# Kernel tuning notes

Measured on AMD Instinct MI355X. Metric: run time of the kernel, lower is better.

The kernel has to match this reference:

```python
import jax, jax.numpy as jnp
import numpy as np

B, T, C, K, TNEI = 16, 1024, 1024, 8, 2
H = int(C * 1.5)  # FeedForward hidden = int(1.5*in_dim)
EPS = 1e-5


def setup_inputs() -> dict:
    key = jax.random.key(0)
    ks = jax.random.split(key, 16)
    ws = C ** -0.5  # fan-in style init scale for projections
    return {
        "x": jax.random.normal(ks[0], (B, T, C), jnp.float32),
        "radj": jax.random.uniform(ks[1], (B, T, K), jnp.float32),
        "inxs": jax.random.randint(ks[2], (B, T, K), 0, T),
        "Wq": jax.random.normal(ks[3], (C, C), jnp.float32) * ws,
        "Wk": jax.random.normal(ks[4], (C, C), jnp.float32) * ws,
        "Wv": jax.random.normal(ks[5], (C, C), jnp.float32) * ws,
        "Wo": jax.random.normal(ks[6], (C, C), jnp.float32) * ws,
        "ln1_g": jnp.ones((C,), jnp.float32),
        "ln1_b": jnp.zeros((C,), jnp.float32),
        "W1": jax.random.normal(ks[7], (C, H), jnp.float32) * ws,
        "b1": jnp.zeros((H,), jnp.float32),
        "W2": jax.random.normal(ks[8], (H, C), jnp.float32) * (H ** -0.5),
        "b2": jnp.zeros((C,), jnp.float32),
        "ln2_g": jnp.ones((C,), jnp.float32),
        "ln2_b": jnp.zeros((C,), jnp.float32),
    }


def _layernorm(x, g, b):
    mu = jnp.mean(x, axis=-1, keepdims=True)
    var = jnp.mean(jnp.square(x - mu), axis=-1, keepdims=True)
    return (x - mu) * jax.lax.rsqrt(var + EPS) * g + b


def reference(x, radj, inxs, Wq, Wk, Wv, Wo, ln1_g, ln1_b, W1, b1, W2, b2, ln2_g, ln2_b):
    scale = 1.0 / jnp.sqrt(jnp.asarray(C, x.dtype))
    gather = jax.vmap(lambda a, i: a[i])  # (T,C),(T,K) -> (T,K,C), vmapped over B

    # MBasicReason: tnei hops of top-k neighbor attention (adjacency-biased)
    h = x
    for _ in range(TNEI):
        q = h @ Wq                                  # (B,T,C)
        kn = gather(h @ Wk, inxs)                   # (B,T,K,C)
        vn = gather(h @ Wv, inxs)                   # (B,T,K,C)
        scores = jnp.einsum('btc,btkc->btk', q, kn) * scale + radj
        attn = jax.nn.softmax(scores, axis=-1)      # (B,T,K); dropout off (eval)
        h = jnp.einsum('btk,btkc->btc', attn, vn) @ Wo

    # residual + LN, FFN, residual + LN
    y = _layernorm(x + jax.nn.relu(h), ln1_g, ln1_b)
    f = jax.nn.relu(y @ W1 + b1) @ W2 + b2
    return _layernorm(y + f, ln2_g, ln2_b)
```

## Files before the change

### kernel.cpp

```cpp
#include <hip/hip_runtime.h>
#include <hip/hip_bf16.h>
#include <cstddef>
#include <cstdint>

#define B_    16
#define T_    1024
#define C_    1024
#define K_    8
#define H_    1536
#define TNEI_ 2
static constexpr float EPS_ = 1e-5f;

typedef __attribute__((ext_vector_type(8))) short bf16x8;
typedef __attribute__((ext_vector_type(4))) float f32x4;

__device__ __forceinline__ float bf2f(unsigned short u) {
    return __uint_as_float(((unsigned)u) << 16);
}
__device__ __forceinline__ unsigned short f2bf(float f) {
    __hip_bfloat16 h = __float2bfloat16(f);
    union { __hip_bfloat16 h; unsigned short u; } cvt;
    cvt.h = h;
    return cvt.u;
}

__device__ __forceinline__ void gload_lds16(const void* g, void* l) {
    __builtin_amdgcn_global_load_lds(
        (const __attribute__((address_space(1))) void*)g,
        (__attribute__((address_space(3))) void*)l,
        16, 0, 0);
}

__global__ __launch_bounds__(256) void f2bf_kernel(
    const float* __restrict__ in, unsigned short* __restrict__ out)
{
    const size_t i = (size_t)blockIdx.x * 256 + threadIdx.x;
    const float4 v = *reinterpret_cast<const float4*>(&in[i * 4]);
    ushort4 o;
    o.x = f2bf(v.x); o.y = f2bf(v.y); o.z = f2bf(v.z); o.w = f2bf(v.w);
    *reinterpret_cast<ushort4*>(&out[i * 4]) = o;
}

__global__ __launch_bounds__(256) void wtrans_kernel(
    const float* __restrict__ W, unsigned short* __restrict__ WT, int R, int Cc)
{
    __shared__ float t[32][33];
    const int c0 = blockIdx.x * 32, r0 = blockIdx.y * 32;
    const int tx = threadIdx.x & 31, ty = threadIdx.x >> 5;
    #pragma unroll
    for (int i = 0; i < 4; ++i)
        t[ty + 8 * i][tx] = W[(size_t)(r0 + ty + 8 * i) * Cc + c0 + tx];
    __syncthreads();
    #pragma unroll
    for (int i = 0; i < 4; ++i)
        WT[(size_t)(c0 + ty + 8 * i) * R + r0 + tx] = f2bf(t[tx][ty + 8 * i]);
}

template <int OUT_BF16, int BIAS, int RELU>
__global__ __launch_bounds__(256) void gemm_bt_kernel(
    const unsigned short* __restrict__ A, const unsigned short* __restrict__ Bt,
    const float* __restrict__ bias, void* __restrict__ Cout,
    int M, int N, int K)
{
    constexpr int BM = 128, BN = 128, BK = 32;
    __shared__ unsigned short smem[2 * (BM * BK + BN * BK)];

    const int tid  = threadIdx.x;
    const int lane = tid & 63;
    const int wid  = tid >> 6;
    const int wm   = wid >> 1, wn = wid & 1;

    const int nwg  = gridDim.x * gridDim.y;
    int bidl = blockIdx.y * gridDim.x + blockIdx.x;
    bidl = (bidl & 7) * (nwg >> 3) + (bidl >> 3);
    const int bx = bidl % gridDim.x;
    const int by = bidl / gridDim.x;
    const int row0 = by * BM;
    const int col0 = bx * BN;

    const int sub = lane >> 2;
    const int kch = lane & 3;

    f32x4 acc[4][4] = {};

    auto stage = [&](int buf, int kt) {
        unsigned short* As = smem + buf * 8192;
        unsigned short* Bs = As + 4096;
        #pragma unroll
        for (int i = 0; i < 2; ++i) {
            const int chunk = i * 4 + wid;
            const int r = chunk * 16 + sub;
            gload_lds16(&A[(size_t)(row0 + r) * K + kt + kch * 8], &As[chunk * 512]);
        }
        #pragma unroll
        for (int i = 0; i < 2; ++i) {
            const int chunk = i * 4 + wid;
            const int r = chunk * 16 + sub;
            gload_lds16(&Bt[(size_t)(col0 + r) * K + kt + kch * 8], &Bs[chunk * 512]);
        }
    };

    auto compute = [&](int buf) {
        const unsigned short* As = smem + buf * 8192;
        const unsigned short* Bs = As + 4096;
        bf16x8 a[4], b[4];
        #pragma unroll
        for (int m = 0; m < 4; ++m) {
            const int r = wm * 64 + m * 16 + (lane & 15);
            a[m] = *reinterpret_cast<const bf16x8*>(&As[r * 32 + (lane >> 4) * 8]);
        }
        #pragma unroll
        for (int n = 0; n < 4; ++n) {
            const int c = wn * 64 + n * 16 + (lane & 15);
            b[n] = *reinterpret_cast<const bf16x8*>(&Bs[c * 32 + (lane >> 4) * 8]);
        }
        #pragma unroll
        for (int m = 0; m < 4; ++m)
            #pragma unroll
            for (int n = 0; n < 4; ++n)
                acc[m][n] = __builtin_amdgcn_mfma_f32_16x16x32_bf16(
                    a[m], b[n], acc[m][n], 0, 0, 0);
    };

    stage(0, 0);
    asm volatile("s_waitcnt vmcnt(0)" ::: "memory");
    __syncthreads();
    int cur = 0;
    for (int kt = BK; kt < K; kt += BK) {
        stage(cur ^ 1, kt);
        compute(cur);
        asm volatile("s_waitcnt vmcnt(0)" ::: "memory");
        __syncthreads();
        cur ^= 1;
    }
    compute(cur);

    if (OUT_BF16) {
        __syncthreads();
        char* tile = (char*)smem;
        #pragma unroll
        for (int m = 0; m < 4; ++m) {
            #pragma unroll
            for (int n = 0; n < 4; ++n) {
                const int cc = wn * 64 + n * 16 + (lane & 15);
                const float bv = BIAS ? bias[col0 + cc] : 0.0f;
                #pragma unroll
                for (int r = 0; r < 4; ++r) {
                    const int rr = wm * 64 + m * 16 + (lane >> 4) * 4 + r;
                    float v = acc[m][n][r] + bv;
                    if (RELU) v = fmaxf(v, 0.0f);
                    const int byte = (rr * 256 + cc * 2) ^ (((rr >> 2) & 3) << 5);
                    *reinterpret_cast<unsigned short*>(tile + byte) = f2bf(v);
                }
            }
        }
        __syncthreads();
        const int cchunk = tid & 15;
        const int rloc   = tid >> 4;
        #pragma unroll
        for (int p = 0; p < 8; ++p) {
            const int rr = p * 16 + rloc;
            const int byte = (rr * 256 + cchunk * 16) ^ (((rr >> 2) & 3) << 5);
            const uint4 v = *reinterpret_cast<const uint4*>(tile + byte);
            *reinterpret_cast<uint4*>(
                &((unsigned short*)Cout)[(size_t)(row0 + rr) * N + col0 + cchunk * 8]) = v;
        }
    } else {
        #pragma unroll
        for (int m = 0; m < 4; ++m) {
            #pragma unroll
            for (int n = 0; n < 4; ++n) {
                const int cg = col0 + wn * 64 + n * 16 + (lane & 15);
                const float bv = BIAS ? bias[cg] : 0.0f;
                #pragma unroll
                for (int r = 0; r < 4; ++r) {
                    const int rg = row0 + wm * 64 + m * 16 + (lane >> 4) * 4 + r;
                    float v = acc[m][n][r] + bv;
                    if (RELU) v = fmaxf(v, 0.0f);
                    ((float*)Cout)[(size_t)rg * N + cg] = v;
                }
            }
        }
    }
}

__global__ __launch_bounds__(256) void attn_kernel(
    const unsigned short* __restrict__ q, const unsigned short* __restrict__ kbuf,
    const unsigned short* __restrict__ vbuf, const int* __restrict__ inxs,
    const float* __restrict__ radj, unsigned short* __restrict__ out)
{
    const int bt  = blockIdx.x;
    const int b   = bt >> 10;
    const int tid = threadIdx.x;
    const float scale = 0.03125f;

    __shared__ int   s_idx[K_];
    __shared__ float s_sc[K_];
    __shared__ float red[K_][4];

    if (tid < K_) s_idx[tid] = inxs[bt * K_ + tid];
    __syncthreads();

    const ushort4 qv = *reinterpret_cast<const ushort4*>(&q[(size_t)bt * C_ + tid * 4]);
    const float qf[4] = { bf2f(qv.x), bf2f(qv.y), bf2f(qv.z), bf2f(qv.w) };

    float part[K_];
    #pragma unroll
    for (int k = 0; k < K_; ++k) {
        const size_t nb = (size_t)b * T_ + s_idx[k];
        const ushort4 kv = *reinterpret_cast<const ushort4*>(&kbuf[nb * C_ + tid * 4]);
        part[k] = qf[0] * bf2f(kv.x) + qf[1] * bf2f(kv.y)
                + qf[2] * bf2f(kv.z) + qf[3] * bf2f(kv.w);
    }

    const int lane = tid & 63, wid = tid >> 6;
    #pragma unroll
    for (int k = 0; k < K_; ++k) {
        float v = part[k];
        #pragma unroll
        for (int off = 32; off; off >>= 1) v += __shfl_xor(v, off);
        if (lane == 0) red[k][wid] = v;
    }
    __syncthreads();
    if (tid < K_) {
        s_sc[tid] = (red[tid][0] + red[tid][1] + red[tid][2] + red[tid][3]) * scale
                    + radj[bt * K_ + tid];
    }
    __syncthreads();

    float m = s_sc[0];
    #pragma unroll
    for (int k = 1; k < K_; ++k) m = fmaxf(m, s_sc[k]);
    float w[K_], wsum = 0.f;
    #pragma unroll
    for (int k = 0; k < K_; ++k) { w[k] = expf(s_sc[k] - m); wsum += w[k]; }
    const float inv = 1.0f / wsum;

    float o[4] = {0.f, 0.f, 0.f, 0.f};
    #pragma unroll
    for (int k = 0; k < K_; ++k) {
        const size_t nb = (size_t)b * T_ + s_idx[k];
        const ushort4 vv = *reinterpret_cast<const ushort4*>(&vbuf[nb * C_ + tid * 4]);
        const float wk = w[k] * inv;
        o[0] = fmaf(wk, bf2f(vv.x), o[0]);
        o[1] = fmaf(wk, bf2f(vv.y), o[1]);
        o[2] = fmaf(wk, bf2f(vv.z), o[2]);
        o[3] = fmaf(wk, bf2f(vv.w), o[3]);
    }
    ushort4 ov;
    ov.x = f2bf(o[0]); ov.y = f2bf(o[1]); ov.z = f2bf(o[2]); ov.w = f2bf(o[3]);
    *reinterpret_cast<ushort4*>(&out[(size_t)bt * C_ + tid * 4]) = ov;
}

template <int RELU, int WB>
__global__ __launch_bounds__(256) void ln_residual_kernel(
    const float* __restrict__ a, const float* __restrict__ bb,
    const float* __restrict__ g, const float* __restrict__ beta,
    float* __restrict__ out, unsigned short* __restrict__ outb)
{
    const int bt  = blockIdx.x;
    const int tid = threadIdx.x;

    const float4 av = *reinterpret_cast<const float4*>(&a[(size_t)bt * C_ + tid * 4]);
    const float4 bv = *reinterpret_cast<const float4*>(&bb[(size_t)bt * C_ + tid * 4]);
    float4 s;
    s.x = av.x + (RELU ? fmaxf(bv.x, 0.f) : bv.x);
    s.y = av.y + (RELU ? fmaxf(bv.y, 0.f) : bv.y);
    s.z = av.z + (RELU ? fmaxf(bv.z, 0.f) : bv.z);
    s.w = av.w + (RELU ? fmaxf(bv.w, 0.f) : bv.w);

    float sum = s.x + s.y + s.z + s.w;
    float sq  = s.x * s.x + s.y * s.y + s.z * s.z + s.w * s.w;

    const int lane = tid & 63, wid = tid >> 6;
    __shared__ float rs[4], rq[4];
    #pragma unroll
    for (int off = 32; off; off >>= 1) {
        sum += __shfl_xor(sum, off);
        sq  += __shfl_xor(sq,  off);
    }
    if (lane == 0) { rs[wid] = sum; rq[wid] = sq; }
    __syncthreads();
    sum = rs[0] + rs[1] + rs[2] + rs[3];
    sq  = rq[0] + rq[1] + rq[2] + rq[3];

    const float mu  = sum * (1.0f / C_);
    const float var = sq * (1.0f / C_) - mu * mu;
    const float r   = rsqrtf(var + EPS_);

    const float4 gv = *reinterpret_cast<const float4*>(&g[tid * 4]);
    const float4 be = *reinterpret_cast<const float4*>(&beta[tid * 4]);
    float4 o;
    o.x = (s.x - mu) * r * gv.x + be.x;
    o.y = (s.y - mu) * r * gv.y + be.y;
    o.z = (s.z - mu) * r * gv.z + be.z;
    o.w = (s.w - mu) * r * gv.w + be.w;
    *reinterpret_cast<float4*>(&out[(size_t)bt * C_ + tid * 4]) = o;
    if (WB) {
        ushort4 ob;
        ob.x = f2bf(o.x); ob.y = f2bf(o.y); ob.z = f2bf(o.z); ob.w = f2bf(o.w);
        *reinterpret_cast<ushort4*>(&outb[(size_t)bt * C_ + tid * 4]) = ob;
    }
}

extern "C" void kernel_launch(void* const* d_in, const int* in_sizes, int n_in,
                              void* d_out, int out_size, void* d_ws, size_t ws_size,
                              hipStream_t stream)
{
    const float* x     = (const float*)d_in[0];
    const float* radj  = (const float*)d_in[1];
    const int*   inxs  = (const int*)  d_in[2];
    const float* Wq    = (const float*)d_in[3];
    const float* Wk    = (const float*)d_in[4];
    const float* Wv    = (const float*)d_in[5];
    const float* Wo    = (const float*)d_in[6];
    const float* ln1_g = (const float*)d_in[7];
    const float* ln1_b = (const float*)d_in[8];
    const float* W1    = (const float*)d_in[9];
    const float* b1    = (const float*)d_in[10];
    const float* W2    = (const float*)d_in[11];
    const float* b2    = (const float*)d_in[12];
    const float* ln2_g = (const float*)d_in[13];
    const float* ln2_b = (const float*)d_in[14];
    float* out = (float*)d_out;

    char* wsb = (char*)d_ws;
    const size_t MB = 1 << 20;
    unsigned short* WqT = (unsigned short*)(wsb + 0 * MB);
    unsigned short* WkT = (unsigned short*)(wsb + 2 * MB);
    unsigned short* WvT = (unsigned short*)(wsb + 4 * MB);
    unsigned short* WoT = (unsigned short*)(wsb + 6 * MB);
    unsigned short* W1T = (unsigned short*)(wsb + 8 * MB);
    unsigned short* W2T = (unsigned short*)(wsb + 11 * MB);
    unsigned short* xb  = (unsigned short*)(wsb + 16 * MB);
    unsigned short* hb  = xb;
    unsigned short* qb  = (unsigned short*)(wsb + 48 * MB);
    unsigned short* kb  = (unsigned short*)(wsb + 80 * MB);
    unsigned short* vb  = (unsigned short*)(wsb + 112 * MB);
    float*          h2  = (float*)(wsb + 144 * MB);
    float*          y   = (float*)(wsb + 48 * MB);
    unsigned short* yb  = (unsigned short*)(wsb + 112 * MB);
    unsigned short* hid = (unsigned short*)(wsb + 144 * MB);
    float*          f   = (float*)(wsb + 192 * MB);

    const int M = B_ * T_;
    const dim3 blk(256);
    const dim3 gC(C_ / 128, M / 128);
    const dim3 gH(H_ / 128, M / 128);

    wtrans_kernel<<<dim3(32, 32), blk, 0, stream>>>(Wq, WqT, C_, C_);
    wtrans_kernel<<<dim3(32, 32), blk, 0, stream>>>(Wk, WkT, C_, C_);
    wtrans_kernel<<<dim3(32, 32), blk, 0, stream>>>(Wv, WvT, C_, C_);
    wtrans_kernel<<<dim3(32, 32), blk, 0, stream>>>(Wo, WoT, C_, C_);
    wtrans_kernel<<<dim3(48, 32), blk, 0, stream>>>(W1, W1T, C_, H_);
    wtrans_kernel<<<dim3(32, 48), blk, 0, stream>>>(W2, W2T, H_, C_);
    f2bf_kernel<<<dim3((size_t)M * C_ / 1024), blk, 0, stream>>>(x, xb);

    for (int hop = 0; hop < TNEI_; ++hop) {
        const unsigned short* hin = (hop == 0) ? xb : hb;
        gemm_bt_kernel<1, 0, 0><<<gC, blk, 0, stream>>>(hin, WqT, nullptr, qb, M, C_, C_);
        gemm_bt_kernel<1, 0, 0><<<gC, blk, 0, stream>>>(hin, WkT, nullptr, kb, M, C_, C_);
        gemm_bt_kernel<1, 0, 0><<<gC, blk, 0, stream>>>(hin, WvT, nullptr, vb, M, C_, C_);
        attn_kernel<<<dim3(M), blk, 0, stream>>>(qb, kb, vb, inxs, radj, qb);
        if (hop == 0)
            gemm_bt_kernel<1, 0, 0><<<gC, blk, 0, stream>>>(qb, WoT, nullptr, hb, M, C_, C_);
        else
            gemm_bt_kernel<0, 0, 0><<<gC, blk, 0, stream>>>(qb, WoT, nullptr, h2, M, C_, C_);
    }

    ln_residual_kernel<1, 1><<<dim3(M), blk, 0, stream>>>(x, h2, ln1_g, ln1_b, y, yb);
    gemm_bt_kernel<1, 1, 1><<<gH, blk, 0, stream>>>(yb,  W1T, b1, hid, M, H_, C_);
    gemm_bt_kernel<0, 1, 0><<<gC, blk, 0, stream>>>(hid, W2T, b2, f,   M, C_, H_);
    ln_residual_kernel<0, 0><<<dim3(M), blk, 0, stream>>>(y, f, ln2_g, ln2_b, out, nullptr);
}
```

Measured before the change: 887.7 us.

## Fuse QKV GEMMs, triple-buffer GEMM with swizzled LDS and priority hints

Concatenates the transposed Wq/Wk/Wv into one weight so Q, K and V come from a single GEMM with N=3072, and the attention kernel reads interleaved qkv rows. The GEMM moves from a double-buffered to a triple-buffered global_load_lds pipeline with partial vmcnt waits, XOR-swizzled LDS chunk placement to reduce bank conflicts, s_setprio around the MFMA block, and launch_bounds(256,2). This aims to cut kernel launches, reuse the A tile across the three projections, and hide load latency better. The cost is more LDS per block and an interleaved qkv layout, which makes the attention gathers stride over larger rows.

New measurement: 801.8 us. 1.11x faster.

```diff
diff --git a/kernel.cpp b/kernel.cpp
--- a/kernel.cpp
+++ b/kernel.cpp
@@ -31,6 +31,15 @@
         16, 0, 0);
 }
 
+#define VMCNT0 asm volatile("s_waitcnt vmcnt(0)" ::: "memory")
+#define VMCNT4 asm volatile("s_waitcnt vmcnt(4)" ::: "memory")
+#define BARRIER do {                                   \
+    __builtin_amdgcn_sched_barrier(0);                 \
+    __builtin_amdgcn_s_barrier();                      \
+    asm volatile("" ::: "memory");                     \
+    __builtin_amdgcn_sched_barrier(0);                 \
+} while (0)
+
 __global__ __launch_bounds__(256) void f2bf_kernel(
     const float* __restrict__ in, unsigned short* __restrict__ out)
 {
@@ -57,13 +66,13 @@
 }
 
 template <int OUT_BF16, int BIAS, int RELU>
-__global__ __launch_bounds__(256) void gemm_bt_kernel(
+__global__ __launch_bounds__(256, 2) void gemm_bt_kernel(
     const unsigned short* __restrict__ A, const unsigned short* __restrict__ Bt,
     const float* __restrict__ bias, void* __restrict__ Cout,
     int M, int N, int K)
 {
-    constexpr int BM = 128, BN = 128, BK = 32;
-    __shared__ unsigned short smem[2 * (BM * BK + BN * BK)];
+    constexpr int BK = 32;
+    __shared__ unsigned short smem[3 * 8192];
 
     const int tid  = threadIdx.x;
     const int lane = tid & 63;
@@ -75,65 +84,80 @@
     bidl = (bidl & 7) * (nwg >> 3) + (bidl >> 3);
     const int bx = bidl % gridDim.x;
     const int by = bidl / gridDim.x;
-    const int row0 = by * BM;
-    const int col0 = bx * BN;
+    const int row0 = by * 128;
+    const int col0 = bx * 128;
+
+    const int NT = K >> 5;
 
     const int sub = lane >> 2;
-    const int kch = lane & 3;
+    const int kk  = (((lane & 3) ^ ((lane >> 3) & 3))) * 8;
 
     f32x4 acc[4][4] = {};
 
-    auto stage = [&](int buf, int kt) {
-        unsigned short* As = smem + buf * 8192;
+    auto stage = [&](int kt, int bufi) {
+        unsigned short* As = smem + bufi * 8192;
         unsigned short* Bs = As + 4096;
         #pragma unroll
         for (int i = 0; i < 2; ++i) {
             const int chunk = i * 4 + wid;
             const int r = chunk * 16 + sub;
-            gload_lds16(&A[(size_t)(row0 + r) * K + kt + kch * 8], &As[chunk * 512]);
+            gload_lds16(&A[(size_t)(row0 + r) * K + kt + kk], &As[chunk * 512]);
         }
         #pragma unroll
         for (int i = 0; i < 2; ++i) {
             const int chunk = i * 4 + wid;
             const int r = chunk * 16 + sub;
-            gload_lds16(&Bt[(size_t)(col0 + r) * K + kt + kch * 8], &Bs[chunk * 512]);
+            gload_lds16(&Bt[(size_t)(col0 + r) * K + kt + kk], &Bs[chunk * 512]);
         }
     };
 
-    auto compute = [&](int buf) {
-        const unsigned short* As = smem + buf * 8192;
+    const int slot = ((lane >> 4) ^ ((lane >> 1) & 3)) * 8;
+    auto loadfrag = [&](int bufi, bf16x8* a, bf16x8* b) {
+        const unsigned short* As = smem + bufi * 8192;
         const unsigned short* Bs = As + 4096;
-        bf16x8 a[4], b[4];
         #pragma unroll
         for (int m = 0; m < 4; ++m) {
             const int r = wm * 64 + m * 16 + (lane & 15);
-            a[m] = *reinterpret_cast<const bf16x8*>(&As[r * 32 + (lane >> 4) * 8]);
+            a[m] = *reinterpret_cast<const bf16x8*>(&As[r * 32 + slot]);
         }
         #pragma unroll
         for (int n = 0; n < 4; ++n) {
             const int c = wn * 64 + n * 16 + (lane & 15);
-            b[n] = *reinterpret_cast<const bf16x8*>(&Bs[c * 32 + (lane >> 4) * 8]);
-        }
+            b[n] = *reinterpret_cast<const bf16x8*>(&Bs[c * 32 + slot]);
+        }
+    };
+
+    auto mfma16 = [&](const bf16x8* a, const bf16x8* b) {
+        __builtin_amdgcn_s_setprio(1);
         #pragma unroll
         for (int m = 0; m < 4; ++m)
             #pragma unroll
             for (int n = 0; n < 4; ++n)
                 acc[m][n] = __builtin_amdgcn_mfma_f32_16x16x32_bf16(
                     a[m], b[n], acc[m][n], 0, 0, 0);
+        __builtin_amdgcn_s_setprio(0);
     };
 
+    bf16x8 fa[4], fb[4];
+
     stage(0, 0);
-    asm volatile("s_waitcnt vmcnt(0)" ::: "memory");
-    __syncthreads();
-    int cur = 0;
-    for (int kt = BK; kt < K; kt += BK) {
-        stage(cur ^ 1, kt);
-        compute(cur);
-        asm volatile("s_waitcnt vmcnt(0)" ::: "memory");
-        __syncthreads();
-        cur ^= 1;
-    }
-    compute(cur);
+    stage(BK, 1);
+    VMCNT4;
+    BARRIER;
+    loadfrag(0, fa, fb);
+
+    int bs = 2, br = 1;
+    for (int t = 0; t < NT; ++t) {
+        if (t + 2 < NT) stage((t + 2) * BK, bs);
+        if (++bs == 3) bs = 0;
+        mfma16(fa, fb);
+        if (t + 1 < NT) {
+            if (t + 2 < NT) { VMCNT4; } else { VMCNT0; }
+            BARRIER;
+            loadfrag(br, fa, fb);
+        }
+        if (++br == 3) br = 0;
+    }
 
     if (OUT_BF16) {
         __syncthreads();
@@ -185,8 +209,7 @@
 }
 
 __global__ __launch_bounds__(256) void attn_kernel(
-    const unsigned short* __restrict__ q, const unsigned short* __restrict__ kbuf,
-    const unsigned short* __restrict__ vbuf, const int* __restrict__ inxs,
+    const unsigned short* __restrict__ qkv, const int* __restrict__ inxs,
     const float* __restrict__ radj, unsigned short* __restrict__ out)
 {
     const int bt  = blockIdx.x;
@@ -201,14 +224,16 @@
     if (tid < K_) s_idx[tid] = inxs[bt * K_ + tid];
     __syncthreads();
 
-    const ushort4 qv = *reinterpret_cast<const ushort4*>(&q[(size_t)bt * C_ + tid * 4]);
+    const ushort4 qv = *reinterpret_cast<const ushort4*>(
+        &qkv[(size_t)bt * 3072 + tid * 4]);
     const float qf[4] = { bf2f(qv.x), bf2f(qv.y), bf2f(qv.z), bf2f(qv.w) };
 
     float part[K_];
     #pragma unroll
     for (int k = 0; k < K_; ++k) {
         const size_t nb = (size_t)b * T_ + s_idx[k];
-        const ushort4 kv = *reinterpret_cast<const ushort4*>(&kbuf[nb * C_ + tid * 4]);
+        const ushort4 kv = *reinterpret_cast<const ushort4*>(
+            &qkv[nb * 3072 + 1024 + tid * 4]);
         part[k] = qf[0] * bf2f(kv.x) + qf[1] * bf2f(kv.y)
                 + qf[2] * bf2f(kv.z) + qf[3] * bf2f(kv.w);
     }
@@ -240,7 +265,8 @@
     #pragma unroll
     for (int k = 0; k < K_; ++k) {
         const size_t nb = (size_t)b * T_ + s_idx[k];
-        const ushort4 vv = *reinterpret_cast<const ushort4*>(&vbuf[nb * C_ + tid * 4]);
+        const ushort4 vv = *reinterpret_cast<const ushort4*>(
+            &qkv[nb * 3072 + 2048 + tid * 4]);
         const float wk = w[k] * inv;
         o[0] = fmaf(wk, bf2f(vv.x), o[0]);
         o[1] = fmaf(wk, bf2f(vv.y), o[1]);
@@ -326,31 +352,29 @@
 
     char* wsb = (char*)d_ws;
     const size_t MB = 1 << 20;
-    unsigned short* WqT = (unsigned short*)(wsb + 0 * MB);
-    unsigned short* WkT = (unsigned short*)(wsb + 2 * MB);
-    unsigned short* WvT = (unsigned short*)(wsb + 4 * MB);
-    unsigned short* WoT = (unsigned short*)(wsb + 6 * MB);
-    unsigned short* W1T = (unsigned short*)(wsb + 8 * MB);
-    unsigned short* W2T = (unsigned short*)(wsb + 11 * MB);
+    unsigned short* WqkvT = (unsigned short*)(wsb + 0 * MB);
+    unsigned short* WoT   = (unsigned short*)(wsb + 6 * MB);
+    unsigned short* W1T   = (unsigned short*)(wsb + 8 * MB);
+    unsigned short* W2T   = (unsigned short*)(wsb + 11 * MB);
     unsigned short* xb  = (unsigned short*)(wsb + 16 * MB);
     unsigned short* hb  = xb;
-    unsigned short* qb  = (unsigned short*)(wsb + 48 * MB);
-    unsigned short* kb  = (unsigned short*)(wsb + 80 * MB);
-    unsigned short* vb  = (unsigned short*)(wsb + 112 * MB);
-    float*          h2  = (float*)(wsb + 144 * MB);
-    float*          y   = (float*)(wsb + 48 * MB);
-    unsigned short* yb  = (unsigned short*)(wsb + 112 * MB);
-    unsigned short* hid = (unsigned short*)(wsb + 144 * MB);
-    float*          f   = (float*)(wsb + 192 * MB);
+    unsigned short* qkv = (unsigned short*)(wsb + 48 * MB);
+    unsigned short* ab  = (unsigned short*)(wsb + 144 * MB);
+    float*          h2  = (float*)(wsb + 48 * MB);
+    float*          y   = (float*)(wsb + 112 * MB);
+    unsigned short* yb  = (unsigned short*)(wsb + 176 * MB);
+    unsigned short* hid = (unsigned short*)(wsb + 208 * MB);
+    float*          f   = (float*)(wsb + 48 * MB);
 
     const int M = B_ * T_;
     const dim3 blk(256);
+    const dim3 gQKV(3 * C_ / 128, M / 128);
     const dim3 gC(C_ / 128, M / 128);
     const dim3 gH(H_ / 128, M / 128);
 
-    wtrans_kernel<<<dim3(32, 32), blk, 0, stream>>>(Wq, WqT, C_, C_);
-    wtrans_kernel<<<dim3(32, 32), blk, 0, stream>>>(Wk, WkT, C_, C_);
-    wtrans_kernel<<<dim3(32, 32), blk, 0, stream>>>(Wv, WvT, C_, C_);
+    wtrans_kernel<<<dim3(32, 32), blk, 0, stream>>>(Wq, WqkvT,                C_, C_);
+    wtrans_kernel<<<dim3(32, 32), blk, 0, stream>>>(Wk, WqkvT + 1024 * 1024,  C_, C_);
+    wtrans_kernel<<<dim3(32, 32), blk, 0, stream>>>(Wv, WqkvT + 2048 * 1024,  C_, C_);
     wtrans_kernel<<<dim3(32, 32), blk, 0, stream>>>(Wo, WoT, C_, C_);
     wtrans_kernel<<<dim3(48, 32), blk, 0, stream>>>(W1, W1T, C_, H_);
     wtrans_kernel<<<dim3(32, 48), blk, 0, stream>>>(W2, W2T, H_, C_);
@@ -358,14 +382,15 @@
 
     for (int hop = 0; hop < TNEI_; ++hop) {
         const unsigned short* hin = (hop == 0) ? xb : hb;
-        gemm_bt_kernel<1, 0, 0><<<gC, blk, 0, stream>>>(hin, WqT, nullptr, qb, M, C_, C_);
-        gemm_bt_kernel<1, 0, 0><<<gC, blk, 0, stream>>>(hin, WkT, nullptr, kb, M, C_, C_);
-        gemm_bt_kernel<1, 0, 0><<<gC, blk, 0, stream>>>(hin, WvT, nullptr, vb, M, C_, C_);
-        attn_kernel<<<dim3(M), blk, 0, stream>>>(qb, kb, vb, inxs, radj, qb);
+        gemm_bt_kernel<1, 0, 0><<<gQKV, blk, 0, stream>>>(hin, WqkvT, nullptr, qkv,
+                                                          M, 3 * C_, C_);
+        attn_kernel<<<dim3(M), blk, 0, stream>>>(qkv, inxs, radj, ab);
         if (hop == 0)
-            gemm_bt_kernel<1, 0, 0><<<gC, blk, 0, stream>>>(qb, WoT, nullptr, hb, M, C_, C_);
+            gemm_bt_kernel<1, 0, 0><<<gC, blk, 0, stream>>>(ab, WoT, nullptr, hb,
+                                                            M, C_, C_);
         else
-            gemm_bt_kernel<0, 0, 0><<<gC, blk, 0, stream>>>(qb, WoT, nullptr, h2, M, C_, C_);
+            gemm_bt_kernel<0, 0, 0><<<gC, blk, 0, stream>>>(ab, WoT, nullptr, h2,
+                                                            M, C_, C_);
     }
 
     ln_residual_kernel<1, 1><<<dim3(M), blk, 0, stream>>>(x, h2, ln1_g, ln1_b, y, yb);
```
